# Kernel tuning notes

Measured on AMD Instinct MI355X. Metric: run time of the kernel, lower is better.

Reference implementation:

```python
import jax, jax.numpy as jnp
import numpy as np

B, N, P, HID = 1024, 30, 16, 128
NR = N * (N - 1)          # 870 directed edges
DR, DE, DO, NT = 3, 5, 6, 5


def _lin(x, w, b):
    return x @ w.T + b


def setup_inputs() -> dict:
    key = jax.random.key(0)
    ks = jax.random.split(key, 24)

    def w(k, o, i):
        return jax.random.normal(k, (o, i), jnp.float32) * 0.05

    def bias(k, o):
        return jax.random.normal(k, (o,), jnp.float32) * 0.05

    return {
        "x": jax.random.normal(ks[0], (B, N, P), jnp.float32),
        "RR": jax.random.normal(ks[1], (B, N, NR), jnp.float32),
        "RS": jax.random.normal(ks[2], (B, N, NR), jnp.float32),
        "RA": jax.random.normal(ks[3], (B, DR, NR), jnp.float32),
        "fr1_w": w(ks[4], HID, 2 * P + DR), "fr1_b": bias(ks[5], HID),
        "fr2_w": w(ks[6], HID // 2, HID),   "fr2_b": bias(ks[7], HID // 2),
        "fr3_w": w(ks[8], DE, HID // 2),    "fr3_b": bias(ks[9], DE),
        "fo1_w": w(ks[10], HID, P + DE),    "fo1_b": bias(ks[11], HID),
        "fo2_w": w(ks[12], HID // 2, HID),  "fo2_b": bias(ks[13], HID // 2),
        "fo3_w": w(ks[14], DO, HID // 2),   "fo3_b": bias(ks[15], DO),
        "fc1_w": w(ks[16], HID, DO * N),    "fc1_b": bias(ks[17], HID),
        "fc2_w": w(ks[18], HID // 2, HID),  "fc2_b": bias(ks[19], HID // 2),
        "fc3_w": w(ks[20], NT, HID // 2),   "fc3_b": bias(ks[21], NT),
    }


def reference(x, RR, RS, RA,
              fr1_w, fr1_b, fr2_w, fr2_b, fr3_w, fr3_b,
              fo1_w, fo1_b, fo2_w, fo2_b, fo3_w, fo3_b,
              fc1_w, fc1_b, fc2_w, fc2_b, fc3_w, fc3_b):
    xt = jnp.swapaxes(x, 1, 2)                       # [B, P, N]
    Orr = jnp.einsum('bpn,bnr->bpr', xt, RR)          # [B, P, Nr]
    Ors = jnp.einsum('bpn,bnr->bpr', xt, RS)          # [B, P, Nr]
    Bm = jnp.concatenate([Orr, Ors, RA], axis=1)      # [B, 2P+Dr, Nr]
    Bm = jnp.swapaxes(Bm, 1, 2)                       # [B, Nr, 2P+Dr]
    h = jax.nn.relu(_lin(Bm, fr1_w, fr1_b))
    h = jax.nn.relu(_lin(h, fr2_w, fr2_b))
    E = jax.nn.relu(_lin(h, fr3_w, fr3_b))            # [B, Nr, De]
    Ebar = jnp.einsum('bre,bnr->ben', E, RR)          # E^T @ RR^T -> [B, De, N]
    C = jnp.concatenate([xt, Ebar], axis=1)           # [B, P+De, N]
    C = jnp.swapaxes(C, 1, 2)                         # [B, N, P+De]
    h = jax.nn.relu(_lin(C, fo1_w, fo1_b))
    h = jax.nn.relu(_lin(h, fo2_w, fo2_b))
    O = jax.nn.relu(_lin(h, fo3_w, fo3_b))            # [B, N, Do]
    f = O.reshape(O.shape[0], -1)                     # [B, Do*N]
    f = jax.nn.relu(_lin(f, fc1_w, fc1_b))
    f = jax.nn.relu(_lin(f, fc2_w, fc2_b))
    return _lin(f, fc3_w, fc3_b)                      # [B, n_targets]
```

## Files before the change

### kernel.cpp

```cpp
#include <hip/hip_runtime.h>

#define B_ 1024
#define N_ 30
#define P_ 16
#define NR_ 870
#define DR_ 3
#define DE_ 5
#define DO_ 6
#define NT_ 5

typedef unsigned short ushort_t;
typedef __attribute__((ext_vector_type(8))) short short8_t;
typedef __attribute__((ext_vector_type(4))) float f32x4;

union Frag { short8_t v; ushort_t u[8]; };

__device__ __forceinline__ float bf2f(ushort_t u) {
    union { unsigned int i; float f; } v; v.i = ((unsigned int)u) << 16; return v.f;
}
__device__ __forceinline__ ushort_t f2bf(float f) {
    union { float f; unsigned int i; } v; v.f = f;
    unsigned int x = v.i;
    return (ushort_t)((x + 0x7FFFu + ((x >> 16) & 1u)) >> 16);
}
__device__ __forceinline__ void split(float v, ushort_t& h, ushort_t& l) {
    h = f2bf(v);
    float r = v - bf2f(h);
    l = f2bf(r);
}
__device__ __forceinline__ f32x4 mfma(short8_t a, short8_t b, f32x4 c) {
    return __builtin_amdgcn_mfma_f32_16x16x32_bf16(a, b, c, 0, 0, 0);
}

__global__ __launch_bounds__(256) void k_prep(
    const float* __restrict__ x,  const float* __restrict__ w1,
    const float* __restrict__ w2, const float* __restrict__ wo1,
    const float* __restrict__ wo2,
    ushort_t* __restrict__ xAh,  ushort_t* __restrict__ xAl,
    ushort_t* __restrict__ w1h,  ushort_t* __restrict__ w1l,
    ushort_t* __restrict__ w2h,  ushort_t* __restrict__ w2l,
    ushort_t* __restrict__ wo1h, ushort_t* __restrict__ wo1l,
    ushort_t* __restrict__ wo2h, ushort_t* __restrict__ wo2l)
{
    const int blk = blockIdx.x, tid = threadIdx.x;
    if (blk < 1024) {
        int b = blk;
        for (int idx = tid; idx < 512; idx += 256) {
            int lane = idx >> 3, j = idx & 7;
            int p = lane & 15, n = (lane >> 4) * 8 + j;
            float v = (n < N_) ? x[(b * N_ + n) * P_ + p] : 0.f;
            ushort_t h_, l_; split(v, h_, l_);
            xAh[b * 512 + idx] = h_; xAl[b * 512 + idx] = l_;
        }
    } else if (blk == 1024) {
        for (int idx = tid; idx < 16 * 512; idx += 256) {
            int f = idx >> 9, eps = idx & 511;
            int lane = eps >> 3, j = eps & 7;
            int mt = f >> 1, kt = f & 1;
            int m = mt * 16 + (lane & 15);
            int k = kt * 32 + (lane >> 4) * 8 + j;
            float v = (k < 35) ? w1[m * 35 + k] : 0.f;
            ushort_t h_, l_; split(v, h_, l_);
            w1h[idx] = h_; w1l[idx] = l_;
        }
    } else if (blk == 1025) {
        for (int idx = tid; idx < 16 * 512; idx += 256) {
            int f = idx >> 9, eps = idx & 511;
            int lane = eps >> 3, j = eps & 7;
            int mt = f >> 2, kt = f & 3;
            int m = mt * 16 + (lane & 15);
            int k = kt * 32 + (lane >> 4) * 8 + j;
            float v = w2[m * 128 + k];
            ushort_t h_, l_; split(v, h_, l_);
            w2h[idx] = h_; w2l[idx] = l_;
        }
    } else if (blk == 1026) {
        for (int idx = tid; idx < 8 * 512; idx += 256) {
            int f = idx >> 9, eps = idx & 511;
            int lane = eps >> 3, j = eps & 7;
            int m = f * 16 + (lane & 15);
            int k = (lane >> 4) * 8 + j;
            float v = (k < 21) ? wo1[m * 21 + k] : 0.f;
            ushort_t h_, l_; split(v, h_, l_);
            wo1h[idx] = h_; wo1l[idx] = l_;
        }
    } else {
        for (int idx = tid; idx < 16 * 512; idx += 256) {
            int f = idx >> 9, eps = idx & 511;
            int lane = eps >> 3, j = eps & 7;
            int mt = f >> 2, kt = f & 3;
            int m = mt * 16 + (lane & 15);
            int k = kt * 32 + (lane >> 4) * 8 + j;
            float v = wo2[m * 128 + k];
            ushort_t h_, l_; split(v, h_, l_);
            wo2h[idx] = h_; wo2l[idx] = l_;
        }
    }
}

__global__ __launch_bounds__(256) void k_edge(
    const float* __restrict__ RR, const float* __restrict__ RS,
    const float* __restrict__ RA,
    const float* __restrict__ b1, const float* __restrict__ b2,
    const float* __restrict__ w3, const float* __restrict__ b3,
    const ushort_t* __restrict__ xAh, const ushort_t* __restrict__ xAl,
    const ushort_t* __restrict__ w1h, const ushort_t* __restrict__ w1l,
    const ushort_t* __restrict__ w2h, const ushort_t* __restrict__ w2l,
    float* __restrict__ Ebar)
{
    const int b   = blockIdx.y;
    const int r0  = blockIdx.x * 64;
    const int tid = threadIdx.x;
    const int lane = tid & 63;
    const int wv   = tid >> 6;
    const int l15  = lane & 15;
    const int q    = lane >> 4;

    __shared__ union {
        ushort_t aT[2][64][72];
        float    h2T[64][68];
    } ua;
    __shared__ ushort_t h1T[2][64][136];
    __shared__ float rrs[30][66];
    __shared__ float Ee[64][6];
    __shared__ float b1s[128], b2s[64];

    if (tid < 128) b1s[tid] = b1[tid];
    if (tid < 64)  b2s[tid] = b2[tid];

    const int eloc = wv * 16 + l15;
    const int r = r0 + eloc;
    const bool rvalid = (r < NR_);

    Frag xh, xl;
    xh.v = ((const short8_t*)xAh)[b * 64 + lane];
    xl.v = ((const short8_t*)xAl)[b * 64 + lane];

    Frag rrh, rrl, rsh, rsl;
    #pragma unroll
    for (int j = 0; j < 8; ++j) {
        int n = q * 8 + j;
        float vr = 0.f, vs = 0.f;
        if (n < N_ && rvalid) {
            vr = RR[(b * N_ + n) * NR_ + r];
            vs = RS[(b * N_ + n) * NR_ + r];
        }
        ushort_t h_, l_;
        split(vr, h_, l_); rrh.u[j] = h_; rrl.u[j] = l_;
        split(vs, h_, l_); rsh.u[j] = h_; rsl.u[j] = l_;
        if (n < N_) rrs[n][eloc] = vr;
    }

    f32x4 aR = {0.f, 0.f, 0.f, 0.f}, aS = {0.f, 0.f, 0.f, 0.f};
    aR = mfma(xh.v, rrh.v, aR); aR = mfma(xl.v, rrh.v, aR); aR = mfma(xh.v, rrl.v, aR);
    aS = mfma(xh.v, rsh.v, aS); aS = mfma(xl.v, rsh.v, aS); aS = mfma(xh.v, rsl.v, aS);

    {
        uint4 z = {0u, 0u, 0u, 0u};
        *(uint4*)&ua.aT[0][eloc][32 + q * 8] = z;
        *(uint4*)&ua.aT[1][eloc][32 + q * 8] = z;
    }
    {
        ushort4 ph, pl;
        ushort_t h_, l_;
        split(aR[0], h_, l_); ph.x = h_; pl.x = l_;
        split(aR[1], h_, l_); ph.y = h_; pl.y = l_;
        split(aR[2], h_, l_); ph.z = h_; pl.z = l_;
        split(aR[3], h_, l_); ph.w = h_; pl.w = l_;
        *(ushort4*)&ua.aT[0][eloc][q * 4] = ph;
        *(ushort4*)&ua.aT[1][eloc][q * 4] = pl;
        split(aS[0], h_, l_); ph.x = h_; pl.x = l_;
        split(aS[1], h_, l_); ph.y = h_; pl.y = l_;
        split(aS[2], h_, l_); ph.z = h_; pl.z = l_;
        split(aS[3], h_, l_); ph.w = h_; pl.w = l_;
        *(ushort4*)&ua.aT[0][eloc][16 + q * 4] = ph;
        *(ushort4*)&ua.aT[1][eloc][16 + q * 4] = pl;
    }
    if (q < DR_) {
        float v = rvalid ? RA[(b * DR_ + q) * NR_ + r] : 0.f;
        ushort_t h_, l_; split(v, h_, l_);
        ua.aT[0][eloc][32 + q] = h_;
        ua.aT[1][eloc][32 + q] = l_;
    }
    __syncthreads();

    {
        short8_t W1hf[2][2], W1lf[2][2];
        #pragma unroll
        for (int mi = 0; mi < 2; ++mi) {
            int mt = wv + mi * 4;
            #pragma unroll
            for (int kt = 0; kt < 2; ++kt) {
                W1hf[mi][kt] = ((const short8_t*)w1h)[(mt * 2 + kt) * 64 + lane];
                W1lf[mi][kt] = ((const short8_t*)w1l)[(mt * 2 + kt) * 64 + lane];
            }
        }
        #pragma unroll
        for (int et = 0; et < 4; ++et) {
            int e = et * 16 + l15;
            short8_t Bh[2], Bl[2];
            #pragma unroll
            for (int kt = 0; kt < 2; ++kt) {
                Bh[kt] = *(const short8_t*)&ua.aT[0][e][kt * 32 + q * 8];
                Bl[kt] = *(const short8_t*)&ua.aT[1][e][kt * 32 + q * 8];
            }
            #pragma unroll
            for (int mi = 0; mi < 2; ++mi) {
                int mt = wv + mi * 4;
                f32x4 acc = {0.f, 0.f, 0.f, 0.f};
                #pragma unroll
                for (int kt = 0; kt < 2; ++kt) {
                    acc = mfma(W1hf[mi][kt], Bh[kt], acc);
                    acc = mfma(W1lf[mi][kt], Bh[kt], acc);
                    acc = mfma(W1hf[mi][kt], Bl[kt], acc);
                }
                ushort4 ph, pl; ushort_t h_, l_;
                float hv;
                hv = fmaxf(acc[0] + b1s[mt * 16 + q * 4 + 0], 0.f); split(hv, h_, l_); ph.x = h_; pl.x = l_;
                hv = fmaxf(acc[1] + b1s[mt * 16 + q * 4 + 1], 0.f); split(hv, h_, l_); ph.y = h_; pl.y = l_;
                hv = fmaxf(acc[2] + b1s[mt * 16 + q * 4 + 2], 0.f); split(hv, h_, l_); ph.z = h_; pl.z = l_;
                hv = fmaxf(acc[3] + b1s[mt * 16 + q * 4 + 3], 0.f); split(hv, h_, l_); ph.w = h_; pl.w = l_;
                *(ushort4*)&h1T[0][e][mt * 16 + q * 4] = ph;
                *(ushort4*)&h1T[1][e][mt * 16 + q * 4] = pl;
            }
        }
    }
    __syncthreads();

    {
        short8_t W2hf[4], W2lf[4];
        #pragma unroll
        for (int kt = 0; kt < 4; ++kt) {
            W2hf[kt] = ((const short8_t*)w2h)[(wv * 4 + kt) * 64 + lane];
            W2lf[kt] = ((const short8_t*)w2l)[(wv * 4 + kt) * 64 + lane];
        }
        #pragma unroll
        for (int et = 0; et < 4; ++et) {
            int e = et * 16 + l15;
            f32x4 acc = {0.f, 0.f, 0.f, 0.f};
            #pragma unroll
            for (int kt = 0; kt < 4; ++kt) {
                short8_t bh = *(const short8_t*)&h1T[0][e][kt * 32 + q * 8];
                short8_t bl = *(const short8_t*)&h1T[1][e][kt * 32 + q * 8];
                acc = mfma(W2hf[kt], bh, acc);
                acc = mfma(W2lf[kt], bh, acc);
                acc = mfma(W2hf[kt], bl, acc);
            }
            float4 st;
            st.x = fmaxf(acc[0] + b2s[wv * 16 + q * 4 + 0], 0.f);
            st.y = fmaxf(acc[1] + b2s[wv * 16 + q * 4 + 1], 0.f);
            st.z = fmaxf(acc[2] + b2s[wv * 16 + q * 4 + 2], 0.f);
            st.w = fmaxf(acc[3] + b2s[wv * 16 + q * 4 + 3], 0.f);
            *(float4*)&ua.h2T[e][wv * 16 + q * 4] = st;
        }
    }
    __syncthreads();

    for (int it = tid; it < 64 * DE_; it += 256) {
        int e = it / DE_, i = it - e * DE_;
        float s = b3[i];
        const float* wr = w3 + i * 64;
        #pragma unroll
        for (int k = 0; k < 64; k += 4) {
            float4 hv = *(const float4*)&ua.h2T[e][k];
            float4 wv4 = *(const float4*)&wr[k];
            s += hv.x * wv4.x + hv.y * wv4.y + hv.z * wv4.z + hv.w * wv4.w;
        }
        Ee[e][i] = ((r0 + e) < NR_) ? fmaxf(s, 0.f) : 0.f;
    }
    __syncthreads();

    if (tid < DE_ * N_) {
        int i = tid / N_, n = tid - i * N_;
        float s = 0.f;
        #pragma unroll
        for (int e = 0; e < 64; ++e) s += Ee[e][i] * rrs[n][e];
        atomicAdd(&Ebar[(b * DE_ + i) * N_ + n], s);
    }
}

__global__ __launch_bounds__(256) void k_node(
    const float* __restrict__ x, const float* __restrict__ Ebar,
    const float* __restrict__ bo1, const float* __restrict__ bo2,
    const float* __restrict__ wo3, const float* __restrict__ bo3,
    const ushort_t* __restrict__ wo1h, const ushort_t* __restrict__ wo1l,
    const ushort_t* __restrict__ wo2h, const ushort_t* __restrict__ wo2l,
    float* __restrict__ f180)
{
    const int b0 = blockIdx.x * 2;
    const int tid = threadIdx.x;
    const int lane = tid & 63;
    const int wv = tid >> 6;
    const int l15 = lane & 15;
    const int q = lane >> 4;

    __shared__ ushort_t cT[2][64][40];
    __shared__ ushort_t h1T[2][64][136];
    __shared__ float h2T[64][68];
    __shared__ float b1s[128], b2s[64];

    if (tid < 128) b1s[tid] = bo1[tid];
    if (tid < 64)  b2s[tid] = bo2[tid];

    for (int idx = tid; idx < 64 * 32; idx += 256) {
        int c = idx >> 5, k = idx & 31;
        int bb = c >> 5, n = c & 31;
        float v = 0.f;
        if (n < N_) {
            if (k < 16)      v = x[((b0 + bb) * N_ + n) * P_ + k];
            else if (k < 21) v = Ebar[((b0 + bb) * DE_ + (k - 16)) * N_ + n];
        }
        ushort_t h_, l_; split(v, h_, l_);
        cT[0][c][k] = h_; cT[1][c][k] = l_;
    }
    __syncthreads();

    {
        short8_t Wh[2], Wl[2];
        #pragma unroll
        for (int mi = 0; mi < 2; ++mi) {
            int mt = wv + mi * 4;
            Wh[mi] = ((const short8_t*)wo1h)[mt * 64 + lane];
            Wl[mi] = ((const short8_t*)wo1l)[mt * 64 + lane];
        }
        #pragma unroll
        for (int et = 0; et < 4; ++et) {
            int c = et * 16 + l15;
            short8_t bh = *(const short8_t*)&cT[0][c][q * 8];
            short8_t bl = *(const short8_t*)&cT[1][c][q * 8];
            #pragma unroll
            for (int mi = 0; mi < 2; ++mi) {
                int mt = wv + mi * 4;
                f32x4 acc = {0.f, 0.f, 0.f, 0.f};
                acc = mfma(Wh[mi], bh, acc);
                acc = mfma(Wl[mi], bh, acc);
                acc = mfma(Wh[mi], bl, acc);
                ushort4 ph, pl; ushort_t h_, l_; float hv;
                hv = fmaxf(acc[0] + b1s[mt * 16 + q * 4 + 0], 0.f); split(hv, h_, l_); ph.x = h_; pl.x = l_;
                hv = fmaxf(acc[1] + b1s[mt * 16 + q * 4 + 1], 0.f); split(hv, h_, l_); ph.y = h_; pl.y = l_;
                hv = fmaxf(acc[2] + b1s[mt * 16 + q * 4 + 2], 0.f); split(hv, h_, l_); ph.z = h_; pl.z = l_;
                hv = fmaxf(acc[3] + b1s[mt * 16 + q * 4 + 3], 0.f); split(hv, h_, l_); ph.w = h_; pl.w = l_;
                *(ushort4*)&h1T[0][c][mt * 16 + q * 4] = ph;
                *(ushort4*)&h1T[1][c][mt * 16 + q * 4] = pl;
            }
        }
    }
    __syncthreads();

    {
        short8_t Wh[4], Wl[4];
        #pragma unroll
        for (int kt = 0; kt < 4; ++kt) {
            Wh[kt] = ((const short8_t*)wo2h)[(wv * 4 + kt) * 64 + lane];
            Wl[kt] = ((const short8_t*)wo2l)[(wv * 4 + kt) * 64 + lane];
        }
        #pragma unroll
        for (int et = 0; et < 4; ++et) {
            int c = et * 16 + l15;
            f32x4 acc = {0.f, 0.f, 0.f, 0.f};
            #pragma unroll
            for (int kt = 0; kt < 4; ++kt) {
                short8_t bh = *(const short8_t*)&h1T[0][c][kt * 32 + q * 8];
                short8_t bl = *(const short8_t*)&h1T[1][c][kt * 32 + q * 8];
                acc = mfma(Wh[kt], bh, acc);
                acc = mfma(Wl[kt], bh, acc);
                acc = mfma(Wh[kt], bl, acc);
            }
            float4 st;
            st.x = fmaxf(acc[0] + b2s[wv * 16 + q * 4 + 0], 0.f);
            st.y = fmaxf(acc[1] + b2s[wv * 16 + q * 4 + 1], 0.f);
            st.z = fmaxf(acc[2] + b2s[wv * 16 + q * 4 + 2], 0.f);
            st.w = fmaxf(acc[3] + b2s[wv * 16 + q * 4 + 3], 0.f);
            *(float4*)&h2T[c][wv * 16 + q * 4] = st;
        }
    }
    __syncthreads();

    for (int it = tid; it < 384; it += 256) {
        int c = it / DO_, i = it - c * DO_;
        if (c < 64) {
            int bb = c >> 5, n = c & 31;
            if (n < N_) {
                float s = bo3[i];
                const float* wr = wo3 + i * 64;
                #pragma unroll
                for (int k = 0; k < 64; k += 4) {
                    float4 hv = *(const float4*)&h2T[c][k];
                    float4 wv4 = *(const float4*)&wr[k];
                    s += hv.x * wv4.x + hv.y * wv4.y + hv.z * wv4.z + hv.w * wv4.w;
                }
                f180[(b0 + bb) * 180 + n * DO_ + i] = fmaxf(s, 0.f);
            }
        }
    }
}

__global__ __launch_bounds__(256) void k_final(
    const float* __restrict__ f180,
    const float* __restrict__ wc1, const float* __restrict__ bc1,
    const float* __restrict__ wc2, const float* __restrict__ bc2,
    const float* __restrict__ wc3, const float* __restrict__ bc3,
    float* __restrict__ out)
{
    const int b0 = blockIdx.x * 2, tid = threadIdx.x;
    __shared__ float fs[2][184];
    __shared__ float h1s[2][128];
    __shared__ float h2s[2][64];

    for (int i = tid; i < 2 * 180; i += 256)
        fs[i / 180][i % 180] = f180[(b0 + i / 180) * 180 + (i % 180)];
    __syncthreads();

    {
        int bl = tid >> 7, j = tid & 127;
        const float* wr = wc1 + j * 180;
        float s = bc1[j];
        #pragma unroll 5
        for (int k = 0; k < 180; k += 4) {
            float4 wv = *(const float4*)&wr[k];
            s += fs[bl][k] * wv.x + fs[bl][k + 1] * wv.y
               + fs[bl][k + 2] * wv.z + fs[bl][k + 3] * wv.w;
        }
        h1s[bl][j] = fmaxf(s, 0.f);
    }
    __syncthreads();

    if (tid < 128) {
        int bl = tid >> 6, j = tid & 63;
        const float* wr = wc2 + j * 128;
        float s = bc2[j];
        #pragma unroll 4
        for (int k = 0; k < 128; k += 4) {
            float4 wv = *(const float4*)&wr[k];
            s += h1s[bl][k] * wv.x + h1s[bl][k + 1] * wv.y
               + h1s[bl][k + 2] * wv.z + h1s[bl][k + 3] * wv.w;
        }
        h2s[bl][j] = fmaxf(s, 0.f);
    }
    __syncthreads();

    if (tid < 10) {
        int bl = tid / 5, t = tid - bl * 5;
        const float* wr = wc3 + t * 64;
        float s = bc3[t];
        #pragma unroll
        for (int k = 0; k < 64; k += 4) {
            float4 wv = *(const float4*)&wr[k];
            s += h2s[bl][k] * wv.x + h2s[bl][k + 1] * wv.y
               + h2s[bl][k + 2] * wv.z + h2s[bl][k + 3] * wv.w;
        }
        out[(b0 + bl) * NT_ + t] = s;
    }
}

extern "C" void kernel_launch(void* const* d_in, const int* in_sizes, int n_in,
                              void* d_out, int out_size, void* d_ws, size_t ws_size,
                              hipStream_t stream)
{
    const float* x    = (const float*)d_in[0];
    const float* RR   = (const float*)d_in[1];
    const float* RS   = (const float*)d_in[2];
    const float* RA   = (const float*)d_in[3];
    const float* fr1w = (const float*)d_in[4];
    const float* fr1b = (const float*)d_in[5];
    const float* fr2w = (const float*)d_in[6];
    const float* fr2b = (const float*)d_in[7];
    const float* fr3w = (const float*)d_in[8];
    const float* fr3b = (const float*)d_in[9];
    const float* fo1w = (const float*)d_in[10];
    const float* fo1b = (const float*)d_in[11];
    const float* fo2w = (const float*)d_in[12];
    const float* fo2b = (const float*)d_in[13];
    const float* fo3w = (const float*)d_in[14];
    const float* fo3b = (const float*)d_in[15];
    const float* fc1w = (const float*)d_in[16];
    const float* fc1b = (const float*)d_in[17];
    const float* fc2w = (const float*)d_in[18];
    const float* fc2b = (const float*)d_in[19];
    const float* fc3w = (const float*)d_in[20];
    const float* fc3b = (const float*)d_in[21];
    float* out = (float*)d_out;

    float* Ebar = (float*)d_ws;
    float* f180 = Ebar + B_ * DE_ * N_;
    ushort_t* base = (ushort_t*)(f180 + B_ * 180);
    ushort_t* xAh  = base;             ushort_t* xAl  = xAh  + 1024 * 512;
    ushort_t* w1h  = xAl  + 1024*512;  ushort_t* w1l  = w1h  + 16 * 512;
    ushort_t* w2h  = w1l  + 16*512;    ushort_t* w2l  = w2h  + 16 * 512;
    ushort_t* wo1h = w2l  + 16*512;    ushort_t* wo1l = wo1h + 8 * 512;
    ushort_t* wo2h = wo1l + 8*512;     ushort_t* wo2l = wo2h + 16 * 512;

    hipMemsetAsync(Ebar, 0, (size_t)B_ * DE_ * N_ * sizeof(float), stream);

    k_prep<<<1028, 256, 0, stream>>>(x, fr1w, fr2w, fo1w, fo2w,
                                     xAh, xAl, w1h, w1l, w2h, w2l,
                                     wo1h, wo1l, wo2h, wo2l);

    dim3 g1(14, B_);
    k_edge<<<g1, 256, 0, stream>>>(RR, RS, RA, fr1b, fr2b, fr3w, fr3b,
                                   xAh, xAl, w1h, w1l, w2h, w2l, Ebar);
    k_node<<<B_ / 2, 256, 0, stream>>>(x, Ebar, fo1b, fo2b, fo3w, fo3b,
                                       wo1h, wo1l, wo2h, wo2l, f180);
    k_final<<<B_ / 2, 256, 0, stream>>>(f180, fc1w, fc1b, fc2w, fc2b,
                                        fc3w, fc3b, out);
}
```

Baseline: 668.8 us.

## Stage RR/RS via coalesced LDS loads and split layer-1 into halves to shrink LDS

The edge kernel now loads RR and RS tiles into shared memory with float2 loads before building MFMA fragments, instead of per-lane strided global reads. The first hidden layer is computed in two 64-column halves, each consumed right away by layer 2 with accumulators kept in registers. This lets h1T shrink to half size and share storage with the RS staging buffer. The aim is better global coalescing and lower LDS use for higher occupancy, at the cost of extra barriers and more live registers.

```diff
diff --git a/kernel.cpp b/kernel.cpp
--- a/kernel.cpp
+++ b/kernel.cpp
@@ -119,142 +119,157 @@
     __shared__ union {
         ushort_t aT[2][64][72];
         float    h2T[64][68];
-    } ua;
-    __shared__ ushort_t h1T[2][64][136];
-    __shared__ float rrs[30][66];
+    } u1;
+    __shared__ union {
+        ushort_t h1T[2][64][72];
+        float    rs[30][70];
+    } u2;
+    __shared__ float rrs[30][70];
     __shared__ float Ee[64][6];
     __shared__ float b1s[128], b2s[64];
 
     if (tid < 128) b1s[tid] = b1[tid];
     if (tid < 64)  b2s[tid] = b2[tid];
+
+    for (int idx = tid; idx < 30 * 32; idx += 256) {
+        int n = idx >> 5, g = idx & 31;
+        int r = r0 + 2 * g;
+        const float* pr = &RR[(b * N_ + n) * NR_];
+        const float* ps = &RS[(b * N_ + n) * NR_];
+        float v0, v1, s0, s1;
+        if (r + 1 < NR_) {
+            float2 a = *(const float2*)&pr[r]; v0 = a.x; v1 = a.y;
+            float2 c = *(const float2*)&ps[r]; s0 = c.x; s1 = c.y;
+        } else {
+            int ra_ = r < NR_ ? r : NR_ - 1;
+            int rb_ = (r + 1) < NR_ ? (r + 1) : NR_ - 1;
+            v0 = pr[ra_]; v1 = pr[rb_]; s0 = ps[ra_]; s1 = ps[rb_];
+        }
+        rrs[n][2 * g] = v0;  rrs[n][2 * g + 1] = v1;
+        u2.rs[n][2 * g] = s0; u2.rs[n][2 * g + 1] = s1;
+    }
+    __syncthreads();
 
     const int eloc = wv * 16 + l15;
     const int r = r0 + eloc;
     const bool rvalid = (r < NR_);
 
-    Frag xh, xl;
-    xh.v = ((const short8_t*)xAh)[b * 64 + lane];
-    xl.v = ((const short8_t*)xAl)[b * 64 + lane];
-
-    Frag rrh, rrl, rsh, rsl;
-    #pragma unroll
-    for (int j = 0; j < 8; ++j) {
-        int n = q * 8 + j;
-        float vr = 0.f, vs = 0.f;
-        if (n < N_ && rvalid) {
-            vr = RR[(b * N_ + n) * NR_ + r];
-            vs = RS[(b * N_ + n) * NR_ + r];
-        }
-        ushort_t h_, l_;
-        split(vr, h_, l_); rrh.u[j] = h_; rrl.u[j] = l_;
-        split(vs, h_, l_); rsh.u[j] = h_; rsl.u[j] = l_;
-        if (n < N_) rrs[n][eloc] = vr;
-    }
-
-    f32x4 aR = {0.f, 0.f, 0.f, 0.f}, aS = {0.f, 0.f, 0.f, 0.f};
-    aR = mfma(xh.v, rrh.v, aR); aR = mfma(xl.v, rrh.v, aR); aR = mfma(xh.v, rrl.v, aR);
-    aS = mfma(xh.v, rsh.v, aS); aS = mfma(xl.v, rsh.v, aS); aS = mfma(xh.v, rsl.v, aS);
-
     {
-        uint4 z = {0u, 0u, 0u, 0u};
-        *(uint4*)&ua.aT[0][eloc][32 + q * 8] = z;
-        *(uint4*)&ua.aT[1][eloc][32 + q * 8] = z;
-    }
-    {
-        ushort4 ph, pl;
-        ushort_t h_, l_;
+        Frag xh, xl;
+        xh.v = ((const short8_t*)xAh)[b * 64 + lane];
+        xl.v = ((const short8_t*)xAl)[b * 64 + lane];
+
+        Frag rrh, rrl, rsh, rsl;
+        #pragma unroll
+        for (int j = 0; j < 8; ++j) {
+            int n = q * 8 + j;
+            float vr = 0.f, vs = 0.f;
+            if (n < N_) { vr = rrs[n][eloc]; vs = u2.rs[n][eloc]; }
+            ushort_t h_, l_;
+            split(vr, h_, l_); rrh.u[j] = h_; rrl.u[j] = l_;
+            split(vs, h_, l_); rsh.u[j] = h_; rsl.u[j] = l_;
+        }
+
+        f32x4 aR = {0.f,0.f,0.f,0.f}, aS = {0.f,0.f,0.f,0.f};
+        aR = mfma(xh.v, rrh.v, aR); aR = mfma(xl.v, rrh.v, aR); aR = mfma(xh.v, rrl.v, aR);
+        aS = mfma(xh.v, rsh.v, aS); aS = mfma(xl.v, rsh.v, aS); aS = mfma(xh.v, rsl.v, aS);
+
+        uint4 z = {0u,0u,0u,0u};
+        *(uint4*)&u1.aT[0][eloc][32 + q * 8] = z;
+        *(uint4*)&u1.aT[1][eloc][32 + q * 8] = z;
+
+        ushort4 ph, pl; ushort_t h_, l_;
         split(aR[0], h_, l_); ph.x = h_; pl.x = l_;
         split(aR[1], h_, l_); ph.y = h_; pl.y = l_;
         split(aR[2], h_, l_); ph.z = h_; pl.z = l_;
         split(aR[3], h_, l_); ph.w = h_; pl.w = l_;
-        *(ushort4*)&ua.aT[0][eloc][q * 4] = ph;
-        *(ushort4*)&ua.aT[1][eloc][q * 4] = pl;
+        *(ushort4*)&u1.aT[0][eloc][q * 4] = ph;
+        *(ushort4*)&u1.aT[1][eloc][q * 4] = pl;
         split(aS[0], h_, l_); ph.x = h_; pl.x = l_;
         split(aS[1], h_, l_); ph.y = h_; pl.y = l_;
         split(aS[2], h_, l_); ph.z = h_; pl.z = l_;
         split(aS[3], h_, l_); ph.w = h_; pl.w = l_;
-        *(ushort4*)&ua.aT[0][eloc][16 + q * 4] = ph;
-        *(ushort4*)&ua.aT[1][eloc][16 + q * 4] = pl;
-    }
-    if (q < DR_) {
-        float v = rvalid ? RA[(b * DR_ + q) * NR_ + r] : 0.f;
-        ushort_t h_, l_; split(v, h_, l_);
-        ua.aT[0][eloc][32 + q] = h_;
-        ua.aT[1][eloc][32 + q] = l_;
-    }
-    __syncthreads();
-
-    {
-        short8_t W1hf[2][2], W1lf[2][2];
-        #pragma unroll
-        for (int mi = 0; mi < 2; ++mi) {
-            int mt = wv + mi * 4;
+        *(ushort4*)&u1.aT[0][eloc][16 + q * 4] = ph;
+        *(ushort4*)&u1.aT[1][eloc][16 + q * 4] = pl;
+
+        if (q < DR_) {
+            float v = rvalid ? RA[(b * DR_ + q) * NR_ + r] : 0.f;
+            split(v, h_, l_);
+            u1.aT[0][eloc][32 + q] = h_;
+            u1.aT[1][eloc][32 + q] = l_;
+        }
+    }
+    __syncthreads();
+
+    short8_t W2hf[4], W2lf[4];
+    #pragma unroll
+    for (int kt = 0; kt < 4; ++kt) {
+        W2hf[kt] = ((const short8_t*)w2h)[(wv * 4 + kt) * 64 + lane];
+        W2lf[kt] = ((const short8_t*)w2l)[(wv * 4 + kt) * 64 + lane];
+    }
+    f32x4 acc2[4];
+    #pragma unroll
+    for (int et = 0; et < 4; ++et) acc2[et] = (f32x4){0.f,0.f,0.f,0.f};
+
+    #pragma unroll
+    for (int hf = 0; hf < 2; ++hf) {
+        {
+            const int mt = hf * 4 + wv;
+            short8_t W1hf_[2], W1lf_[2];
             #pragma unroll
             for (int kt = 0; kt < 2; ++kt) {
-                W1hf[mi][kt] = ((const short8_t*)w1h)[(mt * 2 + kt) * 64 + lane];
-                W1lf[mi][kt] = ((const short8_t*)w1l)[(mt * 2 + kt) * 64 + lane];
-            }
-        }
-        #pragma unroll
-        for (int et = 0; et < 4; ++et) {
-            int e = et * 16 + l15;
-            short8_t Bh[2], Bl[2];
+                W1hf_[kt] = ((const short8_t*)w1h)[(mt * 2 + kt) * 64 + lane];
+                W1lf_[kt] = ((const short8_t*)w1l)[(mt * 2 + kt) * 64 + lane];
+            }
             #pragma unroll
-            for (int kt = 0; kt < 2; ++kt) {
-                Bh[kt] = *(const short8_t*)&ua.aT[0][e][kt * 32 + q * 8];
-                Bl[kt] = *(const short8_t*)&ua.aT[1][e][kt * 32 + q * 8];
-            }
-            #pragma unroll
-            for (int mi = 0; mi < 2; ++mi) {
-                int mt = wv + mi * 4;
-                f32x4 acc = {0.f, 0.f, 0.f, 0.f};
+            for (int et = 0; et < 4; ++et) {
+                int e = et * 16 + l15;
+                f32x4 acc = {0.f,0.f,0.f,0.f};
                 #pragma unroll
                 for (int kt = 0; kt < 2; ++kt) {
-                    acc = mfma(W1hf[mi][kt], Bh[kt], acc);
-                    acc = mfma(W1lf[mi][kt], Bh[kt], acc);
-                    acc = mfma(W1hf[mi][kt], Bl[kt], acc);
+                    short8_t Bh = *(const short8_t*)&u1.aT[0][e][kt * 32 + q * 8];
+                    short8_t Bl = *(const short8_t*)&u1.aT[1][e][kt * 32 + q * 8];
+                    acc = mfma(W1hf_[kt], Bh, acc);
+                    acc = mfma(W1lf_[kt], Bh, acc);
+                    acc = mfma(W1hf_[kt], Bl, acc);
                 }
-                ushort4 ph, pl; ushort_t h_, l_;
-                float hv;
+                ushort4 ph, pl; ushort_t h_, l_; float hv;
                 hv = fmaxf(acc[0] + b1s[mt * 16 + q * 4 + 0], 0.f); split(hv, h_, l_); ph.x = h_; pl.x = l_;
                 hv = fmaxf(acc[1] + b1s[mt * 16 + q * 4 + 1], 0.f); split(hv, h_, l_); ph.y = h_; pl.y = l_;
                 hv = fmaxf(acc[2] + b1s[mt * 16 + q * 4 + 2], 0.f); split(hv, h_, l_); ph.z = h_; pl.z = l_;
                 hv = fmaxf(acc[3] + b1s[mt * 16 + q * 4 + 3], 0.f); split(hv, h_, l_); ph.w = h_; pl.w = l_;
-                *(ushort4*)&h1T[0][e][mt * 16 + q * 4] = ph;
-                *(ushort4*)&h1T[1][e][mt * 16 + q * 4] = pl;
-            }
-        }
-    }
-    __syncthreads();
-
-    {
-        short8_t W2hf[4], W2lf[4];
-        #pragma unroll
-        for (int kt = 0; kt < 4; ++kt) {
-            W2hf[kt] = ((const short8_t*)w2h)[(wv * 4 + kt) * 64 + lane];
-            W2lf[kt] = ((const short8_t*)w2l)[(wv * 4 + kt) * 64 + lane];
-        }
+                *(ushort4*)&u2.h1T[0][e][wv * 16 + q * 4] = ph;
+                *(ushort4*)&u2.h1T[1][e][wv * 16 + q * 4] = pl;
+            }
+        }
+        __syncthreads();
+
         #pragma unroll
         for (int et = 0; et < 4; ++et) {
             int e = et * 16 + l15;
-            f32x4 acc = {0.f, 0.f, 0.f, 0.f};
             #pragma unroll
-            for (int kt = 0; kt < 4; ++kt) {
-                short8_t bh = *(const short8_t*)&h1T[0][e][kt * 32 + q * 8];
-                short8_t bl = *(const short8_t*)&h1T[1][e][kt * 32 + q * 8];
-                acc = mfma(W2hf[kt], bh, acc);
-                acc = mfma(W2lf[kt], bh, acc);
-                acc = mfma(W2hf[kt], bl, acc);
-            }
-            float4 st;
-            st.x = fmaxf(acc[0] + b2s[wv * 16 + q * 4 + 0], 0.f);
-            st.y = fmaxf(acc[1] + b2s[wv * 16 + q * 4 + 1], 0.f);
-            st.z = fmaxf(acc[2] + b2s[wv * 16 + q * 4 + 2], 0.f);
-            st.w = fmaxf(acc[3] + b2s[wv * 16 + q * 4 + 3], 0.f);
-            *(float4*)&ua.h2T[e][wv * 16 + q * 4] = st;
-        }
-    }
-    __syncthreads();
+            for (int ktl = 0; ktl < 2; ++ktl) {
+                short8_t bh = *(const short8_t*)&u2.h1T[0][e][ktl * 32 + q * 8];
+                short8_t bl = *(const short8_t*)&u2.h1T[1][e][ktl * 32 + q * 8];
+                acc2[et] = mfma(W2hf[hf * 2 + ktl], bh, acc2[et]);
+                acc2[et] = mfma(W2lf[hf * 2 + ktl], bh, acc2[et]);
+                acc2[et] = mfma(W2hf[hf * 2 + ktl], bl, acc2[et]);
+            }
+        }
+        if (hf == 1) {
+            #pragma unroll
+            for (int et = 0; et < 4; ++et) {
+                int e = et * 16 + l15;
+                float4 st;
+                st.x = fmaxf(acc2[et][0] + b2s[wv * 16 + q * 4 + 0], 0.f);
+                st.y = fmaxf(acc2[et][1] + b2s[wv * 16 + q * 4 + 1], 0.f);
+                st.z = fmaxf(acc2[et][2] + b2s[wv * 16 + q * 4 + 2], 0.f);
+                st.w = fmaxf(acc2[et][3] + b2s[wv * 16 + q * 4 + 3], 0.f);
+                *(float4*)&u1.h2T[e][wv * 16 + q * 4] = st;
+            }
+        }
+        __syncthreads();
+    }
 
     for (int it = tid; it < 64 * DE_; it += 256) {
         int e = it / DE_, i = it - e * DE_;
@@ -262,7 +277,7 @@
         const float* wr = w3 + i * 64;
         #pragma unroll
         for (int k = 0; k < 64; k += 4) {
-            float4 hv = *(const float4*)&ua.h2T[e][k];
+            float4 hv = *(const float4*)&u1.h2T[e][k];
             float4 wv4 = *(const float4*)&wr[k];
             s += hv.x * wv4.x + hv.y * wv4.y + hv.z * wv4.z + hv.w * wv4.w;
         }
@@ -331,7 +346,7 @@
             #pragma unroll
             for (int mi = 0; mi < 2; ++mi) {
                 int mt = wv + mi * 4;
-                f32x4 acc = {0.f, 0.f, 0.f, 0.f};
+                f32x4 acc = {0.f,0.f,0.f,0.f};
                 acc = mfma(Wh[mi], bh, acc);
                 acc = mfma(Wl[mi], bh, acc);
                 acc = mfma(Wh[mi], bl, acc);
@@ -357,7 +372,7 @@
         #pragma unroll
         for (int et = 0; et < 4; ++et) {
             int c = et * 16 + l15;
-            f32x4 acc = {0.f, 0.f, 0.f, 0.f};
+            f32x4 acc = {0.f,0.f,0.f,0.f};
             #pragma unroll
             for (int kt = 0; kt < 4; ++kt) {
                 short8_t bh = *(const short8_t*)&h1T[0][c][kt * 32 + q * 8];
```

Result: faster. 633.8 us (-5.2%).
